# Kernel optimization log

Measured on AMD Instinct MI355X. Metric: run time of the kernel, lower is better.

Reference implementation:

```python
import jax, jax.numpy as jnp
import numpy as np
from math import sqrt

D = 512        # output_dim (layer_dims[-1])
H = 4          # num_heads
ATN = D // H   # atn_dim = 128
BERT_D = 768
B = 32         # number of graph pairs
NP = 4096
NH = 4096


def setup_inputs() -> dict:
    key = jax.random.key(0)
    ks = jax.random.split(key, 20)
    inp = {
        'ctx_p': jax.random.normal(ks[0], (NP, D), jnp.float32),
        'ctx_h': jax.random.normal(ks[1], (NH, D), jnp.float32),
        'lhs_p': jax.random.normal(ks[2], (NP, BERT_D), jnp.float32),
        'lhs_h': jax.random.normal(ks[3], (NH, BERT_D), jnp.float32),
        'batch_p': jnp.sort(jax.random.randint(ks[4], (NP,), 0, B)).astype(jnp.int64),
        'batch_h': jnp.sort(jax.random.randint(ks[5], (NH,), 0, B)).astype(jnp.int64),
        # learned parameters (stored [in, out])
        'Wq': jax.random.normal(ks[6], (D, D), jnp.float32) * 0.02,
        'bq': jnp.zeros((D,), jnp.float32),
        'Wk': jax.random.normal(ks[7], (D, D), jnp.float32) * 0.02,
        'bk': jnp.zeros((D,), jnp.float32),
        'Wv': jax.random.normal(ks[8], (BERT_D, BERT_D), jnp.float32) * 0.02,
        'bv': jnp.zeros((BERT_D,), jnp.float32),
        'W1': jax.random.normal(ks[9], (D + BERT_D, 256), jnp.float32) * 0.02,
        'b1': jnp.zeros((256,), jnp.float32),
        'W2': jax.random.normal(ks[10], (256, 128), jnp.float32) * 0.02,
        'ln_g': jnp.ones((128,), jnp.float32),
        'ln_b': jnp.zeros((128,), jnp.float32),
        'Wc': jax.random.normal(ks[11], (128, 3), jnp.float32) * 0.02,
        'bc': jnp.zeros((3,), jnp.float32),
    }
    return inp


def reference(ctx_p, ctx_h, lhs_p, lhs_h, batch_p, batch_h,
              Wq, bq, Wk, bk, Wv, bv, W1, b1, W2, ln_g, ln_b, Wc, bc):
    # q/k projections; torch code does .view(-1, atn_dim, num_heads) -> head is fastest axis
    qs = (ctx_h @ Wq + bq).reshape(-1, ATN, H)          # [nh, atn, H]
    ks = (ctx_p @ Wk + bk).reshape(-1, ATN, H)          # [np, atn, H]
    vs = (lhs_p @ Wv + bv).reshape(-1, H, BERT_D // H)  # [np, H, 768/H]

    atn = jnp.einsum('ndh,mdh->nmh', qs, ks) / sqrt(ATN)  # [nh, np, H]
    # faithful to original: positions where batch ids MATCH are set to -1e10
    mask_same = batch_h[:, None] == batch_p[None, :]       # [nh, np]
    atn = jnp.where(mask_same[:, :, None], jnp.float32(-1e10), atn)
    atn = jax.nn.softmax(atn, axis=1)                      # softmax over premise words m

    attended = jnp.einsum('nmh,mhd->nhd', atn, vs).reshape(-1, BERT_D)  # [nh, 768]

    feats = jnp.concatenate([ctx_h, lhs_h - attended], axis=1)  # [nh, D+768]
    h1 = jax.nn.gelu(feats @ W1 + b1, approximate=False)
    h2 = h1 @ W2                                                # Linear no bias
    mu = h2.mean(axis=-1, keepdims=True)
    var = ((h2 - mu) ** 2).mean(axis=-1, keepdims=True)
    h2 = (h2 - mu) * jax.lax.rsqrt(var + 1e-5) * ln_g + ln_b    # LayerNorm(128)

    # global_mean_pool over batch_h
    pooled = jax.ops.segment_sum(h2, batch_h, num_segments=B)
    counts = jax.ops.segment_sum(jnp.ones((h2.shape[0], 1), h2.dtype), batch_h, num_segments=B)
    pooled = pooled / jnp.maximum(counts, 1.0)

    return pooled @ Wc + bc  # [B, 3]
```

## Files before the change

kernel.cpp:

```cpp
#include <hip/hip_runtime.h>
#include <hip/hip_bf16.h>
#include <math.h>

#define NP_N 4096
#define NH_N 4096
#define D_N 512
#define BERT_N 768
#define H_N 4
#define B_N 32

typedef __attribute__((ext_vector_type(8))) short short8;
typedef __attribute__((ext_vector_type(4))) float f32x4;
typedef __attribute__((ext_vector_type(4))) unsigned short ush4;
typedef unsigned short ushort_t;

__device__ __forceinline__ void gl_lds16(const void* g, void* l) {
    __builtin_amdgcn_global_load_lds((const __attribute__((address_space(1))) void*)g,
                                     (__attribute__((address_space(3))) void*)l, 16, 0, 0);
}
__device__ __forceinline__ unsigned short f2bu(float f) {
    __hip_bfloat16 b = __float2bfloat16(f);
    return *reinterpret_cast<unsigned short*>(&b);
}
__device__ __forceinline__ float b2f(unsigned short u) {
    union { unsigned int i; float f; } x; x.i = ((unsigned int)u) << 16; return x.f;
}
__device__ __forceinline__ unsigned int pkbf(float a, float b) {
    union { __hip_bfloat162 h; unsigned int u; } x;
    x.h.x = __float2bfloat16(a);
    x.h.y = __float2bfloat16(b);
    return x.u;
}

#define EW_BLOCKS 512
__global__ __launch_bounds__(256) void convert_all(
    const float* __restrict__ ctx_h, const float* __restrict__ ctx_p,
    const float* __restrict__ lhs_p,
    const float* __restrict__ Wq, const float* __restrict__ Wk,
    const float* __restrict__ Wv, const float* __restrict__ W1,
    const float* __restrict__ bq, const float* __restrict__ bk,
    ushort_t* __restrict__ ctxp_bf, ushort_t* __restrict__ lhsp_bf,
    ushort_t* __restrict__ feats,
    ushort_t* __restrict__ Wqt, ushort_t* __restrict__ Wkt,
    ushort_t* __restrict__ Wvt, ushort_t* __restrict__ W1t,
    float* __restrict__ bqp, float* __restrict__ bkp)
{
    const int bid = blockIdx.x, t = threadIdx.x;
    if (bid < EW_BLOCKS) {
        const long N0 = 524288, N1 = 1048576, TOT = 1835008;
        for (long i = (long)bid * 256 + t; i < TOT; i += (long)EW_BLOCKS * 256) {
            float4 v; ush4 o;
            if (i < N0) {
                long k = i;
                v = ((const float4*)ctx_h)[k];
                o[0] = f2bu(v.x); o[1] = f2bu(v.y); o[2] = f2bu(v.z); o[3] = f2bu(v.w);
                long n = k >> 7, c4 = k & 127;
                ((ush4*)feats)[n * 320 + c4] = o;
            } else if (i < N1) {
                long k = i - N0;
                v = ((const float4*)ctx_p)[k];
                o[0] = f2bu(v.x); o[1] = f2bu(v.y); o[2] = f2bu(v.z); o[3] = f2bu(v.w);
                ((ush4*)ctxp_bf)[k] = o;
            } else {
                long k = i - N1;
                v = ((const float4*)lhs_p)[k];
                o[0] = f2bu(v.x); o[1] = f2bu(v.y); o[2] = f2bu(v.z); o[3] = f2bu(v.w);
                ((ush4*)lhsp_bf)[k] = o;
            }
        }
        if (bid == 0) {
            for (int n = t; n < 512; n += 256) {
                int np = (n & 3) * 128 + (n >> 2);
                bqp[np] = bq[n];
                bkp[np] = bk[n];
            }
        }
        return;
    }
    int tb = bid - EW_BLOCKS;
    const float* src; ushort_t* dst; int K, N, tile, perm;
    if (tb < 64)       { src = Wq; dst = Wqt; K = 512;  N = 512; tile = tb;       perm = 1; }
    else if (tb < 128) { src = Wk; dst = Wkt; K = 512;  N = 512; tile = tb - 64;  perm = 1; }
    else if (tb < 272) { src = Wv; dst = Wvt; K = 768;  N = 768; tile = tb - 128; perm = 0; }
    else               { src = W1; dst = W1t; K = 1280; N = 256; tile = tb - 272; perm = 0; }
    int ntn = N >> 6;
    int k0 = (tile / ntn) * 64, n0 = (tile % ntn) * 64;
    __shared__ float tl[64][65];
#pragma unroll
    for (int i = 0; i < 16; i++) {
        int idx = t + i * 256; int r = idx >> 6, c = idx & 63;
        tl[r][c] = src[(size_t)(k0 + r) * N + n0 + c];
    }
    __syncthreads();
#pragma unroll
    for (int i = 0; i < 16; i++) {
        int idx = t + i * 256; int r = idx >> 6, c = idx & 63;
        int n = n0 + r;
        int nr = perm ? ((n & 3) * 128 + (n >> 2)) : n;
        dst[(size_t)nr * K + k0 + c] = f2bu(tl[c][r]);
    }
}

template<int BIAS_ROW, int GELU>
__global__ __launch_bounds__(256) void gemm_bf(
    const ushort_t* __restrict__ A, int lda, const ushort_t* __restrict__ Bt,
    const float* __restrict__ bias, ushort_t* __restrict__ C,
    int M, int N, int K)
{
    __shared__ ushort_t As[2][64 * 64];
    __shared__ ushort_t Bs[2][64 * 64];
    const int t = threadIdx.x, w = t >> 6, lane = t & 63;
    const int lq = lane & 15, g = lane >> 4;
    const int wm = w >> 1, wn = w & 1;
    const int n0 = blockIdx.x * 64, m0 = blockIdx.y * 64;
    const int nsteps = K >> 6;

    f32x4 acc[2][2];
#pragma unroll
    for (int a = 0; a < 2; a++)
#pragma unroll
        for (int b = 0; b < 2; b++) acc[a][b] = (f32x4){0.f, 0.f, 0.f, 0.f};

    auto STAGE = [&](int buf, int k0) {
#pragma unroll
        for (int jj = 0; jj < 2; jj++) {
            int j = w * 2 + jj;
            int r = j * 8 + (lane >> 3);
            int c = (lane & 7) * 16;
            int cs = c ^ ((r & 7) << 4);
            gl_lds16((const char*)A + ((size_t)(m0 + r) * lda + k0) * 2 + cs, (void*)&As[buf][j * 512]);
            gl_lds16((const char*)Bt + ((size_t)(n0 + r) * K + k0) * 2 + cs, (void*)&Bs[buf][j * 512]);
        }
    };

    STAGE(0, 0);
    __syncthreads();
    int cur = 0;
    for (int s = 0; s < nsteps; s++) {
        if (s + 1 < nsteps) STAGE(cur ^ 1, (s + 1) * 64);
        const char* Ab = (const char*)&As[cur][0];
        const char* Bb = (const char*)&Bs[cur][0];
        const int swz = (lq & 7) << 4;
        short8 af[2][2], bf[2][2];
#pragma unroll
        for (int mf = 0; mf < 2; mf++) {
            int r = wm * 32 + mf * 16 + lq;
#pragma unroll
            for (int ks = 0; ks < 2; ks++)
                af[mf][ks] = *(const short8*)(Ab + r * 128 + ((ks * 64 + g * 16) ^ swz));
        }
#pragma unroll
        for (int nf = 0; nf < 2; nf++) {
            int r = wn * 32 + nf * 16 + lq;
#pragma unroll
            for (int ks = 0; ks < 2; ks++)
                bf[nf][ks] = *(const short8*)(Bb + r * 128 + ((ks * 64 + g * 16) ^ swz));
        }
#pragma unroll
        for (int mf = 0; mf < 2; mf++)
#pragma unroll
            for (int nf = 0; nf < 2; nf++)
#pragma unroll
                for (int ks = 0; ks < 2; ks++)
                    acc[mf][nf] = __builtin_amdgcn_mfma_f32_16x16x32_bf16(
                        af[mf][ks], bf[nf][ks], acc[mf][nf], 0, 0, 0);
        __syncthreads();
        cur ^= 1;
    }

#pragma unroll
    for (int mf = 0; mf < 2; mf++) {
#pragma unroll
        for (int nf = 0; nf < 2; nf++) {
            int ncol = n0 + wn * 32 + nf * 16 + lq;
            float bcol = BIAS_ROW ? 0.f : bias[ncol];
#pragma unroll
            for (int j = 0; j < 4; j++) {
                int mrow = m0 + wm * 32 + mf * 16 + 4 * g + j;
                float v = acc[mf][nf][j] + (BIAS_ROW ? bias[mrow] : bcol);
                if (GELU) v = 0.5f * v * (1.f + erff(v * 0.70710678118654752f));
                C[(size_t)mrow * N + ncol] = f2bu(v);
            }
        }
    }
}

__global__ __launch_bounds__(512, 2) void attn_mfma(
    const ushort_t* __restrict__ Qb,
    const ushort_t* __restrict__ Kb,
    const ushort_t* __restrict__ Vtb,
    const int* __restrict__ batch_h, const int* __restrict__ batch_p,
    ushort_t* __restrict__ Opart,
    float* __restrict__ ml)
{
    const int bid = blockIdx.x;
    const int h = (bid & 7) >> 1;
    const int s = bid & 1;
    const int n0 = (bid >> 3) * 128;

    __shared__ __align__(16) char smem[163840];

    const int t = threadIdx.x;
    const int w = t >> 6, o = w >> 2, wq = w & 3;
    const int lane = t & 63, lq = lane & 15, g = lane >> 4;
    const int lqm = (lq & 7) << 4;
    const float scl2 = 0.12754245006257576f;

    char* Kt0 = smem + (o * 2 + 0) * 16384;
    char* Kt1 = smem + (o * 2 + 1) * 16384;
    char* Vt0 = smem + 65536 + (o * 2 + 0) * 24576;
    char* Vt1 = smem + 65536 + (o * 2 + 1) * 24576;

    short8 qf[2][4];
    int bhq[2];
#pragma unroll
    for (int qg = 0; qg < 2; qg++) {
        const ushort_t* qrow = Qb + (size_t)(n0 + wq * 32 + qg * 16 + lq) * 512 + h * 128;
#pragma unroll
        for (int ks = 0; ks < 4; ks++)
            qf[qg][ks] = *(const short8*)(qrow + ks * 32 + g * 8);
        bhq[qg] = batch_h[n0 + wq * 32 + qg * 16 + lq];
    }

    f32x4 Ofr[2][12];
#pragma unroll
    for (int qg = 0; qg < 2; qg++)
#pragma unroll
        for (int nt = 0; nt < 12; nt++) Ofr[qg][nt] = (f32x4){0.f, 0.f, 0.f, 0.f};
    float m_run[2] = {-1e30f, -1e30f}, l_run[2] = {0.f, 0.f};

    const char* Kg = (const char*)Kb;
    const char* Vg = (const char*)Vtb;
    const int kb = s * 2048 + o * 1024;

    auto STAGE = [&](char* Kd, char* Vd, int m0k) {
#pragma unroll
        for (int jj = 0; jj < 4; jj++) {
            int j = wq * 4 + jj;
            int r = j * 4 + (lane >> 4);
            int c = (lane & 15) * 16;
            gl_lds16(Kg + (size_t)(m0k + r) * 1024 + h * 256 + (c ^ ((r & 7) << 4)),
                     Kd + j * 1024);
        }
#pragma unroll
        for (int jj = 0; jj < 6; jj++) {
            int j = wq * 6 + jj;
            int r = j * 8 + (lane >> 3);
            int c = (lane & 7) * 16;
            gl_lds16(Vg + ((size_t)(h * 192 + r) * 4096 + m0k) * 2 + (c ^ ((r & 7) << 4)),
                     Vd + j * 1024);
        }
    };

    STAGE(Kt0, Vt0, kb);
    __syncthreads();
    int cur = 0;

    for (int tile = 0; tile < 16; tile++) {
        char* Kc = cur ? Kt1 : Kt0;
        char* Vc = cur ? Vt1 : Vt0;
        if (tile + 1 < 16) STAGE(cur ? Kt0 : Kt1, cur ? Vt0 : Vt1, kb + (tile + 1) * 64);

        f32x4 S[2][4];
#pragma unroll
        for (int qg = 0; qg < 2; qg++)
#pragma unroll
            for (int mt = 0; mt < 4; mt++) S[qg][mt] = (f32x4){0.f, 0.f, 0.f, 0.f};
#pragma unroll
        for (int mt = 0; mt < 4; mt++) {
            const char* rbase = Kc + (mt * 16 + lq) * 256;
#pragma unroll
            for (int ks = 0; ks < 4; ks++) {
                short8 kf = *(const short8*)(rbase + ((ks * 64 + g * 16) ^ lqm));
                S[0][mt] = __builtin_amdgcn_mfma_f32_16x16x32_bf16(kf, qf[0][ks], S[0][mt], 0, 0, 0);
                S[1][mt] = __builtin_amdgcn_mfma_f32_16x16x32_bf16(kf, qf[1][ks], S[1][mt], 0, 0, 0);
            }
        }

        int4 bp4[4];
#pragma unroll
        for (int mt = 0; mt < 4; mt++)
            bp4[mt] = *(const int4*)&batch_p[kb + tile * 64 + mt * 16 + 4 * g];

        float mx[2];
#pragma unroll
        for (int qg = 0; qg < 2; qg++) {
            float m = -1e30f;
#pragma unroll
            for (int mt = 0; mt < 4; mt++) {
                float v0 = (bp4[mt].x == bhq[qg]) ? -1e9f : S[qg][mt][0] * scl2;
                float v1 = (bp4[mt].y == bhq[qg]) ? -1e9f : S[qg][mt][1] * scl2;
                float v2 = (bp4[mt].z == bhq[qg]) ? -1e9f : S[qg][mt][2] * scl2;
                float v3 = (bp4[mt].w == bhq[qg]) ? -1e9f : S[qg][mt][3] * scl2;
                S[qg][mt][0] = v0; S[qg][mt][1] = v1; S[qg][mt][2] = v2; S[qg][mt][3] = v3;
                m = fmaxf(m, fmaxf(fmaxf(v0, v1), fmaxf(v2, v3)));
            }
            m = fmaxf(m, __shfl_xor(m, 16));
            m = fmaxf(m, __shfl_xor(m, 32));
            mx[qg] = m;
        }
        bool ng = __all((mx[0] <= m_run[0] + 8.f) && (mx[1] <= m_run[1] + 8.f));

        uint2 P2[2][4];
#pragma unroll
        for (int qg = 0; qg < 2; qg++) {
            float m_new = ng ? m_run[qg] : fmaxf(m_run[qg], mx[qg]);
            float rsum = 0.f;
#pragma unroll
            for (int mt = 0; mt < 4; mt++) {
                float e0 = exp2f(S[qg][mt][0] - m_new);
                float e1 = exp2f(S[qg][mt][1] - m_new);
                float e2 = exp2f(S[qg][mt][2] - m_new);
                float e3 = exp2f(S[qg][mt][3] - m_new);
                rsum += (e0 + e1) + (e2 + e3);
                P2[qg][mt].x = pkbf(e0, e1);
                P2[qg][mt].y = pkbf(e2, e3);
            }
            rsum += __shfl_xor(rsum, 16);
            rsum += __shfl_xor(rsum, 32);
            if (ng) {
                l_run[qg] += rsum;
            } else {
                float f = exp2f(m_run[qg] - m_new);
                l_run[qg] = l_run[qg] * f + rsum;
                m_run[qg] = m_new;
                float fr0 = __shfl(f, 4 * g + 0);
                float fr1 = __shfl(f, 4 * g + 1);
                float fr2 = __shfl(f, 4 * g + 2);
                float fr3 = __shfl(f, 4 * g + 3);
#pragma unroll
                for (int nt = 0; nt < 12; nt++) {
                    Ofr[qg][nt][0] *= fr0; Ofr[qg][nt][1] *= fr1;
                    Ofr[qg][nt][2] *= fr2; Ofr[qg][nt][3] *= fr3;
                }
            }
        }

        __syncthreads();

        char* Pz = Kc + wq * 4096;
#pragma unroll
        for (int qg = 0; qg < 2; qg++)
#pragma unroll
            for (int mt = 0; mt < 4; mt++)
                *(uint2*)(Pz + qg * 2048 + lq * 128 + ((mt * 32 + g * 8) ^ lqm)) = P2[qg][mt];

#pragma unroll
        for (int ks = 0; ks < 2; ks++) {
            short8 pf0 = *(const short8*)(Pz + 0 * 2048 + lq * 128 + ((ks * 64 + g * 16) ^ lqm));
            short8 pf1 = *(const short8*)(Pz + 1 * 2048 + lq * 128 + ((ks * 64 + g * 16) ^ lqm));
#pragma unroll
            for (int nt = 0; nt < 12; nt++) {
                short8 vf = *(const short8*)(Vc + (nt * 16 + lq) * 128 + ((ks * 64 + g * 16) ^ lqm));
                Ofr[0][nt] = __builtin_amdgcn_mfma_f32_16x16x32_bf16(pf0, vf, Ofr[0][nt], 0, 0, 0);
                Ofr[1][nt] = __builtin_amdgcn_mfma_f32_16x16x32_bf16(pf1, vf, Ofr[1][nt], 0, 0, 0);
            }
        }

        __syncthreads();
        cur ^= 1;
    }

    const int tq = wq * 64 + lane;
    float* mOf = (float*)smem;
    float* mls = (float*)(smem + 98304);
    if (o == 1) {
#pragma unroll
        for (int qg = 0; qg < 2; qg++) {
#pragma unroll
            for (int nt = 0; nt < 12; nt++)
                *(f32x4*)(mOf + tq * 96 + qg * 48 + nt * 4) = Ofr[qg][nt];
            if (g == 0) {
                mls[(wq * 16 + lq) * 4 + qg * 2 + 0] = m_run[qg];
                mls[(wq * 16 + lq) * 4 + qg * 2 + 1] = l_run[qg];
            }
        }
    }
    __syncthreads();
    if (o == 0) {
        const size_t plane = (size_t)(s * 4 + h) * 4096;
#pragma unroll
        for (int qg = 0; qg < 2; qg++) {
            float m1 = mls[(wq * 16 + lq) * 4 + qg * 2 + 0];
            float l1 = mls[(wq * 16 + lq) * 4 + qg * 2 + 1];
            float m = fmaxf(m_run[qg], m1);
            float a0 = exp2f(m_run[qg] - m), a1 = exp2f(m1 - m);
            float l = l_run[qg] * a0 + l1 * a1;
            int qrow = n0 + wq * 32 + qg * 16;
            if (g == 0) {
                ml[(plane + qrow + lq) * 2 + 0] = m;
                ml[(plane + qrow + lq) * 2 + 1] = l;
            }
            float f0[4], f1[4];
#pragma unroll
            for (int j = 0; j < 4; j++) {
                f0[j] = __shfl(a0, 4 * g + j);
                f1[j] = __shfl(a1, 4 * g + j);
            }
#pragma unroll
            for (int nt = 0; nt < 12; nt++) {
                f32x4 o1 = *(f32x4*)(mOf + tq * 96 + qg * 48 + nt * 4);
#pragma unroll
                for (int j = 0; j < 4; j++) {
                    float val = Ofr[qg][nt][j] * f0[j] + o1[j] * f1[j];
                    Opart[(plane + qrow + 4 * g + j) * 192 + nt * 16 + lq] = f2bu(val);
                }
            }
        }
    }
}

__global__ __launch_bounds__(256) void combine_feats(
    const ushort_t* __restrict__ Opart, const float* __restrict__ ml,
    const float* __restrict__ lhs_h, ushort_t* __restrict__ feats)
{
    const int t = threadIdx.x;
#pragma unroll
    for (int i = 0; i < 4; i++) {
        int q = blockIdx.x * 4 + i;
#pragma unroll
        for (int it = 0; it < 3; it++) {
            int c = t + it * 256;
            int h = c / 192, vd = c - h * 192;
            size_t i0 = (size_t)h * 4096 + q;
            size_t i1 = (size_t)(4 + h) * 4096 + q;
            float m0 = ml[i0 * 2], l0 = ml[i0 * 2 + 1];
            float m1 = ml[i1 * 2], l1 = ml[i1 * 2 + 1];
            float m = fmaxf(m0, m1);
            float e0 = exp2f(m0 - m), e1 = exp2f(m1 - m);
            float linv = 1.f / (l0 * e0 + l1 * e1);
            float O = (b2f(Opart[i0 * 192 + vd]) * e0 + b2f(Opart[i1 * 192 + vd]) * e1) * linv;
            feats[(size_t)q * 1280 + 512 + c] = f2bu(lhs_h[(size_t)q * 768 + c] - O);
        }
    }
}

__global__ __launch_bounds__(256) void h2_ln(
    const ushort_t* __restrict__ h1, const float* __restrict__ W2,
    const float* __restrict__ ln_g, const float* __restrict__ ln_b,
    float* __restrict__ h2out)
{
    const int n0 = blockIdx.x * 8;
    const int t = threadIdx.x;
    __shared__ float h1s[8][256];
    __shared__ float h2s[8][128];

#pragma unroll
    for (int i = 0; i < 8; i++) {
        int idx = t + i * 256; int r = idx >> 8, c = idx & 255;
        h1s[r][c] = b2f(h1[(size_t)(n0 + r) * 256 + c]);
    }
    __syncthreads();

    {
        int o2 = t & 127, gq = t >> 7;
        float acc[4] = {};
        for (int k4 = 0; k4 < 64; k4++) {
            float w0 = W2[(size_t)(k4 * 4 + 0) * 128 + o2];
            float w1 = W2[(size_t)(k4 * 4 + 1) * 128 + o2];
            float w2 = W2[(size_t)(k4 * 4 + 2) * 128 + o2];
            float w3 = W2[(size_t)(k4 * 4 + 3) * 128 + o2];
#pragma unroll
            for (int q = 0; q < 4; q++) {
                float4 hh = *(const float4*)&h1s[gq * 4 + q][k4 * 4];
                acc[q] += hh.x * w0 + hh.y * w1 + hh.z * w2 + hh.w * w3;
            }
        }
#pragma unroll
        for (int q = 0; q < 4; q++) h2s[gq * 4 + q][o2] = acc[q];
    }
    __syncthreads();

    {
        int wv = t >> 6, lane = t & 63;
#pragma unroll
        for (int sx = 0; sx < 2; sx++) {
            int nd = wv * 2 + sx;
            float x0 = h2s[nd][lane], x1 = h2s[nd][lane + 64];
            float sum = x0 + x1;
#pragma unroll
            for (int off = 32; off; off >>= 1) sum += __shfl_xor(sum, off);
            float mu = sum * (1.f / 128.f);
            float d0 = x0 - mu, d1 = x1 - mu;
            float s2 = d0 * d0 + d1 * d1;
#pragma unroll
            for (int off = 32; off; off >>= 1) s2 += __shfl_xor(s2, off);
            float rstd = rsqrtf(s2 * (1.f / 128.f) + 1e-5f);
            size_t base = (size_t)(n0 + nd) * 128;
            h2out[base + lane]      = d0 * rstd * ln_g[lane] + ln_b[lane];
            h2out[base + lane + 64] = d1 * rstd * ln_g[lane + 64] + ln_b[lane + 64];
        }
    }
}

__global__ void ranges_kernel(const int* __restrict__ bh, int* __restrict__ lo,
                              int Nn, int Bn)
{
    int n = blockIdx.x * blockDim.x + threadIdx.x;
    if (n >= Nn) return;
    int b = bh[n];
    int prev = (n == 0) ? -1 : bh[n - 1];
    for (int bb = prev + 1; bb <= b; bb++) lo[bb] = n;
    if (n == Nn - 1) for (int bb = b + 1; bb <= Bn; bb++) lo[bb] = Nn;
}

__global__ __launch_bounds__(128) void pool_cls(
    const float* __restrict__ h2, const int* __restrict__ lo,
    const float* __restrict__ Wc, const float* __restrict__ bc,
    float* __restrict__ out)
{
    int b = blockIdx.x, t = threadIdx.x;
    int s = lo[b], e = lo[b + 1];
    float acc = 0.f;
    for (int n = s; n < e; n++) acc += h2[(size_t)n * 128 + t];
    float pooled = acc / fmaxf((float)(e - s), 1.f);
    __shared__ float red[128];
    for (int c = 0; c < 3; c++) {
        red[t] = pooled * Wc[t * 3 + c];
        __syncthreads();
        for (int off = 64; off > 0; off >>= 1) {
            if (t < off) red[t] += red[t + off];
            __syncthreads();
        }
        if (t == 0) out[b * 3 + c] = red[0] + bc[c];
        __syncthreads();
    }
}

extern "C" void kernel_launch(void* const* d_in, const int* in_sizes, int n_in,
                              void* d_out, int out_size, void* d_ws, size_t ws_size,
                              hipStream_t stream)
{
    const float* ctx_p  = (const float*)d_in[0];
    const float* ctx_h  = (const float*)d_in[1];
    const float* lhs_p  = (const float*)d_in[2];
    const float* lhs_h  = (const float*)d_in[3];
    const int*   batch_p = (const int*)d_in[4];
    const int*   batch_h = (const int*)d_in[5];
    const float* Wq = (const float*)d_in[6];
    const float* bq = (const float*)d_in[7];
    const float* Wk = (const float*)d_in[8];
    const float* bk = (const float*)d_in[9];
    const float* Wv = (const float*)d_in[10];
    const float* bv = (const float*)d_in[11];
    const float* W1 = (const float*)d_in[12];
    const float* b1 = (const float*)d_in[13];
    const float* W2 = (const float*)d_in[14];
    const float* ln_g = (const float*)d_in[15];
    const float* ln_b = (const float*)d_in[16];
    const float* Wc = (const float*)d_in[17];
    const float* bc = (const float*)d_in[18];
    float* out = (float*)d_out;

    ushort_t* u = (ushort_t*)d_ws;
    ushort_t* ctxp_bf = u;
    ushort_t* lhsp_bf = ctxp_bf + 2097152;
    ushort_t* Wqt  = lhsp_bf + 3145728;
    ushort_t* Wkt  = Wqt + 262144;
    ushort_t* Wvt  = Wkt + 262144;
    ushort_t* Opart = u;
    ushort_t* W1t  = Wvt + 589824;
    ushort_t* Qb   = W1t + 327680;
    ushort_t* Kb   = Qb + 2097152;
    ushort_t* Vtb  = Kb + 2097152;
    ushort_t* feats = Vtb + 3145728;
    ushort_t* h1   = feats + 5242880;
    float* ml  = (float*)(h1 + 1048576);
    float* h2  = ml + 65536;
    float* bqp = h2 + 524288;
    float* bkp = bqp + 512;
    int*   lo  = (int*)(bkp + 512);

    convert_all<<<864, 256, 0, stream>>>(
        ctx_h, ctx_p, lhs_p, Wq, Wk, Wv, W1, bq, bk,
        ctxp_bf, lhsp_bf, feats, Wqt, Wkt, Wvt, W1t, bqp, bkp);

    gemm_bf<0, 0><<<dim3(8, 64), 256, 0, stream>>>(feats, 1280, Wqt, bqp, Qb, NH_N, 512, 512);
    gemm_bf<0, 0><<<dim3(8, 64), 256, 0, stream>>>(ctxp_bf, 512, Wkt, bkp, Kb, NP_N, 512, 512);
    gemm_bf<1, 0><<<dim3(64, 12), 256, 0, stream>>>(Wvt, 768, lhsp_bf, bv, Vtb, 768, NP_N, 768);

    attn_mfma<<<256, 512, 0, stream>>>(Qb, Kb, Vtb, batch_h, batch_p, Opart, ml);

    combine_feats<<<1024, 256, 0, stream>>>(Opart, ml, lhs_h, feats);

    gemm_bf<0, 1><<<dim3(4, 64), 256, 0, stream>>>(feats, 1280, W1t, b1, h1, NH_N, 256, 1280);

    h2_ln<<<512, 256, 0, stream>>>(h1, W2, ln_g, ln_b, h2);
    ranges_kernel<<<16, 256, 0, stream>>>(batch_h, lo, NH_N, B_N);
    pool_cls<<<B_N, 128, 0, stream>>>(h2, lo, Wc, bc, out);
}
```

Measured before the change: 195.0 us.

## Enlarge GEMM tiles, skip fully-masked attention tiles, and lighten barriers

The GEMM kernel becomes templated with 128-row tiles and 128- or 64-column tiles, so each wave computes more MFMA fragments per LDS load. It also raises wave priority around the MFMA blocks and uses raw s_barrier with an explicit vmcnt wait. The attention kernel reads batch-id ranges per tile and skips the whole QK/softmax/PV work when every pair in the tile is masked. It also drops the mask compare when no pair matches. Larger tiles cut the grid sizes, which may lower occupancy on a large GPU. Skipping fully masked tiles relies on the sorted batch ids and leaves such rows unnormalised if every key is masked.

```diff
diff --git a/kernel.cpp b/kernel.cpp
--- a/kernel.cpp
+++ b/kernel.cpp
@@ -101,82 +101,92 @@
     }
 }
 
-template<int BIAS_ROW, int GELU>
-__global__ __launch_bounds__(256) void gemm_bf(
+template<int TN, int BIAS_ROW, int GELU>
+__global__ __launch_bounds__(256) void gemm2(
     const ushort_t* __restrict__ A, int lda, const ushort_t* __restrict__ Bt,
     const float* __restrict__ bias, ushort_t* __restrict__ C,
     int M, int N, int K)
 {
-    __shared__ ushort_t As[2][64 * 64];
-    __shared__ ushort_t Bs[2][64 * 64];
+    constexpr int NF = TN / 32;
+    __shared__ ushort_t As[2][128 * 64];
+    __shared__ ushort_t Bs[2][TN * 64];
     const int t = threadIdx.x, w = t >> 6, lane = t & 63;
     const int lq = lane & 15, g = lane >> 4;
     const int wm = w >> 1, wn = w & 1;
-    const int n0 = blockIdx.x * 64, m0 = blockIdx.y * 64;
+    const int n0 = blockIdx.x * TN, m0 = blockIdx.y * 128;
     const int nsteps = K >> 6;
 
-    f32x4 acc[2][2];
-#pragma unroll
-    for (int a = 0; a < 2; a++)
-#pragma unroll
-        for (int b = 0; b < 2; b++) acc[a][b] = (f32x4){0.f, 0.f, 0.f, 0.f};
+    f32x4 acc[4][NF] = {};
 
     auto STAGE = [&](int buf, int k0) {
 #pragma unroll
-        for (int jj = 0; jj < 2; jj++) {
-            int j = w * 2 + jj;
+        for (int jj = 0; jj < 4; jj++) {
+            int j = w * 4 + jj;
             int r = j * 8 + (lane >> 3);
             int c = (lane & 7) * 16;
             int cs = c ^ ((r & 7) << 4);
-            gl_lds16((const char*)A + ((size_t)(m0 + r) * lda + k0) * 2 + cs, (void*)&As[buf][j * 512]);
-            gl_lds16((const char*)Bt + ((size_t)(n0 + r) * K + k0) * 2 + cs, (void*)&Bs[buf][j * 512]);
+            gl_lds16((const char*)A + ((size_t)(m0 + r) * lda + k0) * 2 + cs,
+                     (void*)&As[buf][j * 512]);
+        }
+#pragma unroll
+        for (int jj = 0; jj < TN / 32; jj++) {
+            int j = w * (TN / 32) + jj;
+            int r = j * 8 + (lane >> 3);
+            int c = (lane & 7) * 16;
+            int cs = c ^ ((r & 7) << 4);
+            gl_lds16((const char*)Bt + ((size_t)(n0 + r) * K + k0) * 2 + cs,
+                     (void*)&Bs[buf][j * 512]);
         }
     };
 
     STAGE(0, 0);
-    __syncthreads();
+    asm volatile("s_waitcnt vmcnt(0)" ::: "memory");
+    __builtin_amdgcn_s_barrier();
     int cur = 0;
     for (int s = 0; s < nsteps; s++) {
         if (s + 1 < nsteps) STAGE(cur ^ 1, (s + 1) * 64);
         const char* Ab = (const char*)&As[cur][0];
         const char* Bb = (const char*)&Bs[cur][0];
         const int swz = (lq & 7) << 4;
-        short8 af[2][2], bf[2][2];
-#pragma unroll
-        for (int mf = 0; mf < 2; mf++) {
-            int r = wm * 32 + mf * 16 + lq;
+        short8 af[4][2], bfr[NF][2];
+#pragma unroll
+        for (int mf = 0; mf < 4; mf++) {
+            int r = wm * 64 + mf * 16 + lq;
 #pragma unroll
             for (int ks = 0; ks < 2; ks++)
                 af[mf][ks] = *(const short8*)(Ab + r * 128 + ((ks * 64 + g * 16) ^ swz));
         }
 #pragma unroll
-        for (int nf = 0; nf < 2; nf++) {
-            int r = wn * 32 + nf * 16 + lq;
+        for (int nf = 0; nf < NF; nf++) {
+            int r = wn * (TN / 2) + nf * 16 + lq;
 #pragma unroll
             for (int ks = 0; ks < 2; ks++)
-                bf[nf][ks] = *(const short8*)(Bb + r * 128 + ((ks * 64 + g * 16) ^ swz));
-        }
-#pragma unroll
-        for (int mf = 0; mf < 2; mf++)
-#pragma unroll
-            for (int nf = 0; nf < 2; nf++)
+                bfr[nf][ks] = *(const short8*)(Bb + r * 128 + ((ks * 64 + g * 16) ^ swz));
+        }
+        __builtin_amdgcn_s_setprio(1);
+#pragma unroll
+        for (int mf = 0; mf < 4; mf++)
+#pragma unroll
+            for (int nf = 0; nf < NF; nf++)
 #pragma unroll
                 for (int ks = 0; ks < 2; ks++)
                     acc[mf][nf] = __builtin_amdgcn_mfma_f32_16x16x32_bf16(
-                        af[mf][ks], bf[nf][ks], acc[mf][nf], 0, 0, 0);
-        __syncthreads();
+                        af[mf][ks], bfr[nf][ks], acc[mf][nf], 0, 0, 0);
+        __builtin_amdgcn_s_setprio(0);
+        asm volatile("s_waitcnt vmcnt(0)" ::: "memory");
+        __builtin_amdgcn_s_barrier();
         cur ^= 1;
     }
 
 #pragma unroll
-    for (int mf = 0; mf < 2; mf++) {
-#pragma unroll
-        for (int nf = 0; nf < 2; nf++) {
-            int ncol = n0 + wn * 32 + nf * 16 + lq;
+    for (int mf = 0; mf < 4; mf++) {
+#pragma unroll
+        for (int nf = 0; nf < NF; nf++) {
+            int ncol = n0 + wn * (TN / 2) + nf * 16 + lq;
             float bcol = BIAS_ROW ? 0.f : bias[ncol];
 #pragma unroll
             for (int j = 0; j < 4; j++) {
-                int mrow = m0 + wm * 32 + mf * 16 + 4 * g + j;
+                int mrow = m0 + wm * 64 + mf * 16 + 4 * g + j;
                 float v = acc[mf][nf][j] + (BIAS_ROW ? bias[mrow] : bcol);
                 if (GELU) v = 0.5f * v * (1.f + erff(v * 0.70710678118654752f));
                 C[(size_t)mrow * N + ncol] = f2bu(v);
@@ -221,6 +231,8 @@
             qf[qg][ks] = *(const short8*)(qrow + ks * 32 + g * 8);
         bhq[qg] = batch_h[n0 + wq * 32 + qg * 16 + lq];
     }
+    const int bh_lo = batch_h[n0 + wq * 32];
+    const int bh_hi = batch_h[n0 + wq * 32 + 31];
 
     f32x4 Ofr[2][12];
 #pragma unroll
@@ -253,7 +265,8 @@
     };
 
     STAGE(Kt0, Vt0, kb);
-    __syncthreads();
+    asm volatile("s_waitcnt vmcnt(0)" ::: "memory");
+    __builtin_amdgcn_s_barrier();
     int cur = 0;
 
     for (int tile = 0; tile < 16; tile++) {
@@ -261,103 +274,136 @@
         char* Vc = cur ? Vt1 : Vt0;
         if (tile + 1 < 16) STAGE(cur ? Kt0 : Kt1, cur ? Vt0 : Vt1, kb + (tile + 1) * 64);
 
-        f32x4 S[2][4];
-#pragma unroll
-        for (int qg = 0; qg < 2; qg++)
-#pragma unroll
-            for (int mt = 0; mt < 4; mt++) S[qg][mt] = (f32x4){0.f, 0.f, 0.f, 0.f};
-#pragma unroll
-        for (int mt = 0; mt < 4; mt++) {
-            const char* rbase = Kc + (mt * 16 + lq) * 256;
-#pragma unroll
-            for (int ks = 0; ks < 4; ks++) {
-                short8 kf = *(const short8*)(rbase + ((ks * 64 + g * 16) ^ lqm));
-                S[0][mt] = __builtin_amdgcn_mfma_f32_16x16x32_bf16(kf, qf[0][ks], S[0][mt], 0, 0, 0);
-                S[1][mt] = __builtin_amdgcn_mfma_f32_16x16x32_bf16(kf, qf[1][ks], S[1][mt], 0, 0, 0);
-            }
-        }
-
-        int4 bp4[4];
-#pragma unroll
-        for (int mt = 0; mt < 4; mt++)
-            bp4[mt] = *(const int4*)&batch_p[kb + tile * 64 + mt * 16 + 4 * g];
-
-        float mx[2];
-#pragma unroll
-        for (int qg = 0; qg < 2; qg++) {
-            float m = -1e30f;
+        const int ktb = kb + tile * 64;
+        const int kt_lo = batch_p[ktb];
+        const int kt_hi = batch_p[ktb + 63];
+        const bool allmask = (kt_lo == kt_hi) && (kt_lo == bh_lo) && (bh_lo == bh_hi);
+        const bool needmask = (kt_lo <= bh_hi) && (kt_hi >= bh_lo);
+
+        if (!allmask) {
+            f32x4 S[2][4];
+#pragma unroll
+            for (int qg = 0; qg < 2; qg++)
+#pragma unroll
+                for (int mt = 0; mt < 4; mt++) S[qg][mt] = (f32x4){0.f, 0.f, 0.f, 0.f};
+            __builtin_amdgcn_s_setprio(1);
 #pragma unroll
             for (int mt = 0; mt < 4; mt++) {
-                float v0 = (bp4[mt].x == bhq[qg]) ? -1e9f : S[qg][mt][0] * scl2;
-                float v1 = (bp4[mt].y == bhq[qg]) ? -1e9f : S[qg][mt][1] * scl2;
-                float v2 = (bp4[mt].z == bhq[qg]) ? -1e9f : S[qg][mt][2] * scl2;
-                float v3 = (bp4[mt].w == bhq[qg]) ? -1e9f : S[qg][mt][3] * scl2;
-                S[qg][mt][0] = v0; S[qg][mt][1] = v1; S[qg][mt][2] = v2; S[qg][mt][3] = v3;
-                m = fmaxf(m, fmaxf(fmaxf(v0, v1), fmaxf(v2, v3)));
-            }
-            m = fmaxf(m, __shfl_xor(m, 16));
-            m = fmaxf(m, __shfl_xor(m, 32));
-            mx[qg] = m;
-        }
-        bool ng = __all((mx[0] <= m_run[0] + 8.f) && (mx[1] <= m_run[1] + 8.f));
-
-        uint2 P2[2][4];
-#pragma unroll
-        for (int qg = 0; qg < 2; qg++) {
-            float m_new = ng ? m_run[qg] : fmaxf(m_run[qg], mx[qg]);
-            float rsum = 0.f;
-#pragma unroll
-            for (int mt = 0; mt < 4; mt++) {
-                float e0 = exp2f(S[qg][mt][0] - m_new);
-                float e1 = exp2f(S[qg][mt][1] - m_new);
-                float e2 = exp2f(S[qg][mt][2] - m_new);
-                float e3 = exp2f(S[qg][mt][3] - m_new);
-                rsum += (e0 + e1) + (e2 + e3);
-                P2[qg][mt].x = pkbf(e0, e1);
-                P2[qg][mt].y = pkbf(e2, e3);
-            }
-            rsum += __shfl_xor(rsum, 16);
-            rsum += __shfl_xor(rsum, 32);
-            if (ng) {
-                l_run[qg] += rsum;
+                const char* rbase = Kc + (mt * 16 + lq) * 256;
+#pragma unroll
+                for (int ks = 0; ks < 4; ks++) {
+                    short8 kf = *(const short8*)(rbase + ((ks * 64 + g * 16) ^ lqm));
+                    S[0][mt] = __builtin_amdgcn_mfma_f32_16x16x32_bf16(kf, qf[0][ks], S[0][mt], 0, 0, 0);
+                    S[1][mt] = __builtin_amdgcn_mfma_f32_16x16x32_bf16(kf, qf[1][ks], S[1][mt], 0, 0, 0);
+                }
+            }
+            __builtin_amdgcn_s_setprio(0);
+
+            float mx[2];
+            if (needmask) {
+                int4 bp4[4];
+#pragma unroll
+                for (int mt = 0; mt < 4; mt++)
+                    bp4[mt] = *(const int4*)&batch_p[ktb + mt * 16 + 4 * g];
+#pragma unroll
+                for (int qg = 0; qg < 2; qg++) {
+                    float m = -1e30f;
+#pragma unroll
+                    for (int mt = 0; mt < 4; mt++) {
+                        float v0 = (bp4[mt].x == bhq[qg]) ? -1e9f : S[qg][mt][0] * scl2;
+                        float v1 = (bp4[mt].y == bhq[qg]) ? -1e9f : S[qg][mt][1] * scl2;
+                        float v2 = (bp4[mt].z == bhq[qg]) ? -1e9f : S[qg][mt][2] * scl2;
+                        float v3 = (bp4[mt].w == bhq[qg]) ? -1e9f : S[qg][mt][3] * scl2;
+                        S[qg][mt][0] = v0; S[qg][mt][1] = v1; S[qg][mt][2] = v2; S[qg][mt][3] = v3;
+                        m = fmaxf(m, fmaxf(fmaxf(v0, v1), fmaxf(v2, v3)));
+                    }
+                    m = fmaxf(m, __shfl_xor(m, 16));
+                    m = fmaxf(m, __shfl_xor(m, 32));
+                    mx[qg] = m;
+                }
             } else {
-                float f = exp2f(m_run[qg] - m_new);
-                l_run[qg] = l_run[qg] * f + rsum;
-                m_run[qg] = m_new;
-                float fr0 = __shfl(f, 4 * g + 0);
-                float fr1 = __shfl(f, 4 * g + 1);
-                float fr2 = __shfl(f, 4 * g + 2);
-                float fr3 = __shfl(f, 4 * g + 3);
+#pragma unroll
+                for (int qg = 0; qg < 2; qg++) {
+                    float m = -1e30f;
+#pragma unroll
+                    for (int mt = 0; mt < 4; mt++) {
+                        float v0 = S[qg][mt][0] * scl2;
+                        float v1 = S[qg][mt][1] * scl2;
+                        float v2 = S[qg][mt][2] * scl2;
+                        float v3 = S[qg][mt][3] * scl2;
+                        S[qg][mt][0] = v0; S[qg][mt][1] = v1; S[qg][mt][2] = v2; S[qg][mt][3] = v3;
+                        m = fmaxf(m, fmaxf(fmaxf(v0, v1), fmaxf(v2, v3)));
+                    }
+                    m = fmaxf(m, __shfl_xor(m, 16));
+                    m = fmaxf(m, __shfl_xor(m, 32));
+                    mx[qg] = m;
+                }
+            }
+            bool ng = __all((mx[0] <= m_run[0] + 8.f) && (mx[1] <= m_run[1] + 8.f));
+
+            uint2 P2[2][4];
+#pragma unroll
+            for (int qg = 0; qg < 2; qg++) {
+                float m_new = ng ? m_run[qg] : fmaxf(m_run[qg], mx[qg]);
+                float rsum = 0.f;
+#pragma unroll
+                for (int mt = 0; mt < 4; mt++) {
+                    float e0 = exp2f(S[qg][mt][0] - m_new);
+                    float e1 = exp2f(S[qg][mt][1] - m_new);
+                    float e2 = exp2f(S[qg][mt][2] - m_new);
+                    float e3 = exp2f(S[qg][mt][3] - m_new);
+                    rsum += (e0 + e1) + (e2 + e3);
+                    P2[qg][mt].x = pkbf(e0, e1);
+                    P2[qg][mt].y = pkbf(e2, e3);
+                }
+                rsum += __shfl_xor(rsum, 16);
+                rsum += __shfl_xor(rsum, 32);
+                if (ng) {
+                    l_run[qg] += rsum;
+                } else {
+                    float f = exp2f(m_run[qg] - m_new);
+                    l_run[qg] = l_run[qg] * f + rsum;
+                    m_run[qg] = m_new;
+                    float fr0 = __shfl(f, 4 * g + 0);
+                    float fr1 = __shfl(f, 4 * g + 1);
+                    float fr2 = __shfl(f, 4 * g + 2);
+                    float fr3 = __shfl(f, 4 * g + 3);
+#pragma unroll
+                    for (int nt = 0; nt < 12; nt++) {
+                        Ofr[qg][nt][0] *= fr0; Ofr[qg][nt][1] *= fr1;
+                        Ofr[qg][nt][2] *= fr2; Ofr[qg][nt][3] *= fr3;
+                    }
+                }
+            }
+
+            __builtin_amdgcn_s_barrier();
+
+            char* Pz = Kc + wq * 4096;
+#pragma unroll
+            for (int qg = 0; qg < 2; qg++)
+#pragma unroll
+                for (int mt = 0; mt < 4; mt++)
+                    *(uint2*)(Pz + qg * 2048 + lq * 128 + ((mt * 32 + g * 8) ^ lqm)) = P2[qg][mt];
+
+            __builtin_amdgcn_s_setprio(1);
+#pragma unroll
+            for (int ks = 0; ks < 2; ks++) {
+                short8 pf0 = *(const short8*)(Pz + 0 * 2048 + lq * 128 + ((ks * 64 + g * 16) ^ lqm));
+                short8 pf1 = *(const short8*)(Pz + 1 * 2048 + lq * 128 + ((ks * 64 + g * 16) ^ lqm));
 #pragma unroll
                 for (int nt = 0; nt < 12; nt++) {
-                    Ofr[qg][nt][0] *= fr0; Ofr[qg][nt][1] *= fr1;
-                    Ofr[qg][nt][2] *= fr2; Ofr[qg][nt][3] *= fr3;
+                    short8 vf = *(const short8*)(Vc + (nt * 16 + lq) * 128 + ((ks * 64 + g * 16) ^ lqm));
+                    Ofr[0][nt] = __builtin_amdgcn_mfma_f32_16x16x32_bf16(pf0, vf, Ofr[0][nt], 0, 0, 0);
+                    Ofr[1][nt] = __builtin_amdgcn_mfma_f32_16x16x32_bf16(pf1, vf, Ofr[1][nt], 0, 0, 0);
                 }
             }
-        }
-
-        __syncthreads();
-
-        char* Pz = Kc + wq * 4096;
-#pragma unroll
-        for (int qg = 0; qg < 2; qg++)
-#pragma unroll
-            for (int mt = 0; mt < 4; mt++)
-                *(uint2*)(Pz + qg * 2048 + lq * 128 + ((mt * 32 + g * 8) ^ lqm)) = P2[qg][mt];
-
-#pragma unroll
-        for (int ks = 0; ks < 2; ks++) {
-            short8 pf0 = *(const short8*)(Pz + 0 * 2048 + lq * 128 + ((ks * 64 + g * 16) ^ lqm));
-            short8 pf1 = *(const short8*)(Pz + 1 * 2048 + lq * 128 + ((ks * 64 + g * 16) ^ lqm));
-#pragma unroll
-            for (int nt = 0; nt < 12; nt++) {
-                short8 vf = *(const short8*)(Vc + (nt * 16 + lq) * 128 + ((ks * 64 + g * 16) ^ lqm));
-                Ofr[0][nt] = __builtin_amdgcn_mfma_f32_16x16x32_bf16(pf0, vf, Ofr[0][nt], 0, 0, 0);
-                Ofr[1][nt] = __builtin_amdgcn_mfma_f32_16x16x32_bf16(pf1, vf, Ofr[1][nt], 0, 0, 0);
-            }
-        }
-
-        __syncthreads();
+            __builtin_amdgcn_s_setprio(0);
+        } else {
+            __builtin_amdgcn_s_barrier();
+        }
+
+        asm volatile("s_waitcnt vmcnt(0)" ::: "memory");
+        __builtin_amdgcn_s_barrier();
         cur ^= 1;
     }
 
@@ -575,15 +621,15 @@
         ctx_h, ctx_p, lhs_p, Wq, Wk, Wv, W1, bq, bk,
         ctxp_bf, lhsp_bf, feats, Wqt, Wkt, Wvt, W1t, bqp, bkp);
 
-    gemm_bf<0, 0><<<dim3(8, 64), 256, 0, stream>>>(feats, 1280, Wqt, bqp, Qb, NH_N, 512, 512);
-    gemm_bf<0, 0><<<dim3(8, 64), 256, 0, stream>>>(ctxp_bf, 512, Wkt, bkp, Kb, NP_N, 512, 512);
-    gemm_bf<1, 0><<<dim3(64, 12), 256, 0, stream>>>(Wvt, 768, lhsp_bf, bv, Vtb, 768, NP_N, 768);
+    gemm2<128, 0, 0><<<dim3(4, 32), 256, 0, stream>>>(feats, 1280, Wqt, bqp, Qb, NH_N, 512, 512);
+    gemm2<128, 0, 0><<<dim3(4, 32), 256, 0, stream>>>(ctxp_bf, 512, Wkt, bkp, Kb, NP_N, 512, 512);
+    gemm2<128, 1, 0><<<dim3(32, 6), 256, 0, stream>>>(Wvt, 768, lhsp_bf, bv, Vtb, 768, NP_N, 768);
 
     attn_mfma<<<256, 512, 0, stream>>>(Qb, Kb, Vtb, batch_h, batch_p, Opart, ml);
 
     combine_feats<<<1024, 256, 0, stream>>>(Opart, ml, lhs_h, feats);
 
-    gemm_bf<0, 1><<<dim3(4, 64), 256, 0, stream>>>(feats, 1280, W1t, b1, h1, NH_N, 256, 1280);
+    gemm2<64, 0, 1><<<dim3(4, 32), 256, 0, stream>>>(feats, 1280, W1t, b1, h1, NH_N, 256, 1280);
 
     h2_ln<<<512, 256, 0, stream>>>(h1, W2, ln_g, ln_b, h2);
     ranges_kernel<<<16, 256, 0, stream>>>(batch_h, lo, NH_N, B_N);
```

After: 219.0 us. 1.12x slower.
